# Performance work log

Hardware: AMD Instinct MI355X
Metric: run time of the kernel (lower is better)

Reference implementation:

```python
import jax, jax.numpy as jnp
import numpy as np

N_NODES = 50000
N_EDGES = 800000
N_GRAPHS = 128
IN_DIM = 100
HID = 256
STEPS = 5


def setup_inputs() -> dict:
    key = jax.random.key(0)
    ks = jax.random.split(key, 24)
    s = 0.05
    inp = {
        'x': jax.random.normal(ks[0], (N_NODES, IN_DIM), jnp.float32),
        'edge_index': jax.random.randint(ks[1], (2, N_EDGES), 0, N_NODES, jnp.int32),
        'batch': jnp.sort(jax.random.randint(ks[2], (N_NODES,), 0, N_GRAPHS, jnp.int32)),
        # input projection
        'W_in': jax.random.normal(ks[3], (IN_DIM, HID), jnp.float32) * s,
        'b_in': jnp.zeros((HID,), jnp.float32),
        # GatedGraphConv per-step weights [steps, HID, HID]
        'ggc_w': jax.random.normal(ks[4], (STEPS, HID, HID), jnp.float32) * s,
        # GRUCell params (torch layout: rows = [r, z, n] chunks)
        'W_ih': jax.random.normal(ks[5], (3 * HID, HID), jnp.float32) * s,
        'W_hh': jax.random.normal(ks[6], (3 * HID, HID), jnp.float32) * s,
        'b_ih': jnp.zeros((3 * HID,), jnp.float32),
        'b_hh': jnp.zeros((3 * HID,), jnp.float32),
        # attention MLP: HID -> HID//2 -> 1 (sigmoid)
        'Wa1': jax.random.normal(ks[7], (HID, HID // 2), jnp.float32) * s,
        'ba1': jnp.zeros((HID // 2,), jnp.float32),
        'Wa2': jax.random.normal(ks[8], (HID // 2, 1), jnp.float32) * s,
        'ba2': jnp.zeros((1,), jnp.float32),
        # classifier: 2*HID -> HID -> HID//2 -> 2
        'Wc1': jax.random.normal(ks[9], (2 * HID, HID), jnp.float32) * s,
        'bc1': jnp.zeros((HID,), jnp.float32),
        'Wc2': jax.random.normal(ks[10], (HID, HID // 2), jnp.float32) * s,
        'bc2': jnp.zeros((HID // 2,), jnp.float32),
        'Wc3': jax.random.normal(ks[11], (HID // 2, 2), jnp.float32) * s,
        'bc3': jnp.zeros((2,), jnp.float32),
    }
    return inp


def _forward(x, edge_index, batch, W_in, b_in, ggc_w, W_ih, W_hh, b_ih, b_hh,
             Wa1, ba1, Wa2, ba2, Wc1, bc1, Wc2, bc2, Wc3, bc3):
    src, dst = edge_index[0], edge_index[1]
    # input projection + relu
    h = jax.nn.relu(x @ W_in + b_in)  # [N, HID]

    def ggc_step(h, w):
        m = h @ w                                   # [N, HID]
        agg = jax.ops.segment_sum(m[src], dst, num_segments=N_NODES)  # scatter-add
        gi = agg @ W_ih.T + b_ih                    # [N, 3*HID]
        gh = h @ W_hh.T + b_hh
        i_r, i_z, i_n = jnp.split(gi, 3, axis=-1)
        h_r, h_z, h_n = jnp.split(gh, 3, axis=-1)
        r = jax.nn.sigmoid(i_r + h_r)
        z = jax.nn.sigmoid(i_z + h_z)
        n = jnp.tanh(i_n + r * h_n)
        return (1.0 - z) * n + z * h, None

    h, _ = jax.lax.scan(ggc_step, h, ggc_w)
    h = jax.nn.relu(h)

    # attention weights per node (dropout is identity at eval)
    a = jax.nn.sigmoid(jax.nn.relu(h @ Wa1 + ba1) @ Wa2 + ba2)[:, 0]  # [N]
    wx = h * a[:, None]

    counts = jax.ops.segment_sum(jnp.ones((N_NODES,), h.dtype), batch, num_segments=N_GRAPHS)
    mean_p = jax.ops.segment_sum(wx, batch, num_segments=N_GRAPHS) / jnp.maximum(counts, 1.0)[:, None]
    max_p = jax.ops.segment_max(wx, batch, num_segments=N_GRAPHS)
    max_p = jnp.where(counts[:, None] > 0, max_p, 0.0)
    g = jnp.concatenate([mean_p, max_p], axis=1)  # [G, 2*HID]

    g = jax.nn.relu(g @ Wc1 + bc1)
    g = jax.nn.relu(g @ Wc2 + bc2)
    preds = g @ Wc3 + bc3
    return preds, a


def reference(x, edge_index, batch, W_in, b_in, ggc_w, W_ih, W_hh, b_ih, b_hh,
              Wa1, ba1, Wa2, ba2, Wc1, bc1, Wc2, bc2, Wc3, bc3):
    return _forward(x, edge_index, batch, W_in, b_in, ggc_w, W_ih, W_hh, b_ih, b_hh,
                    Wa1, ba1, Wa2, ba2, Wc1, bc1, Wc2, bc2, Wc3, bc3)
```

## Files before the change

### kernel.cpp

```cpp
#include <hip/hip_runtime.h>
#include <cstddef>

#define NN 50000
#define NE 800000
#define NG 128
#define IND 100
#define HID 256
#define NSTEPS 5
#define PCH 8

typedef __attribute__((ext_vector_type(8))) short bf16x8;
typedef __attribute__((ext_vector_type(4))) float f32x4;

__device__ __forceinline__ float b2f(unsigned h) { return __uint_as_float(h << 16); }
__device__ __forceinline__ unsigned short f2b(float f) {
    unsigned u = __float_as_uint(f);
    unsigned r = (u + 0x7FFFu + ((u >> 16) & 1u)) >> 16;
    return (unsigned short)r;
}
__device__ __forceinline__ float sigm(float x) { return 1.f / (1.f + __expf(-x)); }
__device__ __forceinline__ float tanh_fast(float x) { return 1.f - 2.f / (1.f + __expf(2.f * x)); }

#define LSTR 40
__global__ __launch_bounds__(256) void gemm_bf16(const unsigned short* __restrict__ A,
                                                 const unsigned short* __restrict__ Bt,
                                                 const float* __restrict__ bias, int act,
                                                 unsigned short* __restrict__ C,
                                                 unsigned short* __restrict__ Clo,
                                                 int M, int N, int K,
                                                 size_t btz, size_t cz)
{
    Bt += (size_t)blockIdx.z * btz;
    C  += (size_t)blockIdx.z * cz;
    __shared__ unsigned short As[128 * LSTR];
    __shared__ unsigned short Bs[128 * LSTR];
    const int tid  = threadIdx.x;
    const int row0 = blockIdx.y * 128;
    const int col0 = blockIdx.x * 128;
    const int wave = tid >> 6, lane = tid & 63;
    const int wm = wave >> 1, wn = wave & 1;
    const int lr = lane & 15, q = lane >> 4;
    const int r_st = tid >> 2;
    const int ks   = tid & 3;

    f32x4 acc[4][4];
    #pragma unroll
    for (int i = 0; i < 4; ++i)
        #pragma unroll
        for (int j = 0; j < 4; ++j) acc[i][j] = (f32x4){0.f, 0.f, 0.f, 0.f};

    for (int k0 = 0; k0 < K; k0 += 32) {
        #pragma unroll
        for (int it = 0; it < 2; ++it) {
            int r  = r_st + it * 64;
            int ga = min(row0 + r, M - 1);
            uint4 av = *(const uint4*)(A + (size_t)ga * K + k0 + ks * 8);
            *(uint4*)(As + r * LSTR + ks * 8) = av;
            uint4 bv = *(const uint4*)(Bt + (size_t)(col0 + r) * K + k0 + ks * 8);
            *(uint4*)(Bs + r * LSTR + ks * 8) = bv;
        }
        __syncthreads();
        bf16x8 af[4], bfr[4];
        #pragma unroll
        for (int i = 0; i < 4; ++i)
            af[i]  = *(const bf16x8*)(As + (wm * 64 + i * 16 + lr) * LSTR + q * 8);
        #pragma unroll
        for (int j = 0; j < 4; ++j)
            bfr[j] = *(const bf16x8*)(Bs + (wn * 64 + j * 16 + lr) * LSTR + q * 8);
        #pragma unroll
        for (int i = 0; i < 4; ++i)
            #pragma unroll
            for (int j = 0; j < 4; ++j)
                acc[i][j] = __builtin_amdgcn_mfma_f32_16x16x32_bf16(af[i], bfr[j], acc[i][j], 0, 0, 0);
        __syncthreads();
    }
    #pragma unroll
    for (int i = 0; i < 4; ++i) {
        int rbase = row0 + wm * 64 + i * 16 + q * 4;
        #pragma unroll
        for (int j = 0; j < 4; ++j) {
            int col = col0 + wn * 64 + j * 16 + lr;
            if (col >= N) continue;
            float badd = bias ? bias[col] : 0.f;
            #pragma unroll
            for (int r = 0; r < 4; ++r) {
                int row = rbase + r;
                if (row < M) {
                    float v = acc[i][j][r] + badd;
                    if (act) v = fmaxf(v, 0.f);
                    unsigned short hi = f2b(v);
                    C[(size_t)row * N + col] = hi;
                    if (Clo) Clo[(size_t)row * N + col] = f2b(v - b2f(hi));
                }
            }
        }
    }
}

__global__ __launch_bounds__(256, 4) void gru_mfma(const unsigned short* __restrict__ agg,
                                                   const unsigned short* __restrict__ hbf,
                                                   const unsigned short* __restrict__ hlo,
                                                   unsigned short* __restrict__ hbfo,
                                                   unsigned short* __restrict__ hloo,
                                                   const unsigned short* __restrict__ Wgi,
                                                   const unsigned short* __restrict__ Wgh,
                                                   const float* __restrict__ bih,
                                                   const float* __restrict__ bhh,
                                                   int M, int dorelu)
{
    __shared__ unsigned short Sa[2][64 * LSTR];
    __shared__ unsigned short Sh[2][64 * LSTR];
    const int tid  = threadIdx.x;
    const int row0 = blockIdx.y * 64;
    const int col0 = blockIdx.x * 64;
    const int wave = tid >> 6, lane = tid & 63;
    const int lr = lane & 15, q = lane >> 4;
    const int cw = col0 + wave * 16;
    const int r_st = tid >> 2, ks = tid & 3;

    f32x4 acc[4][4];
    #pragma unroll
    for (int g = 0; g < 4; ++g)
        #pragma unroll
        for (int i = 0; i < 4; ++i) acc[g][i] = (f32x4){0.f, 0.f, 0.f, 0.f};

    const int ga = min(row0 + r_st, M - 1);
    const size_t ab = (size_t)ga * HID + ks * 8;
    {
        uint4 a0 = *(const uint4*)(agg + ab);
        uint4 h0 = *(const uint4*)(hbf + ab);
        *(uint4*)(Sa[0] + r_st * LSTR + ks * 8) = a0;
        *(uint4*)(Sh[0] + r_st * LSTR + ks * 8) = h0;
    }
    uint4 pa = *(const uint4*)(agg + ab + 32);
    uint4 ph = *(const uint4*)(hbf + ab + 32);

    #pragma unroll
    for (int kk = 0; kk < 8; ++kk) {
        const int cur = kk & 1;
        const int k0 = kk * 32;
        __syncthreads();
        if (kk < 7) {
            *(uint4*)(Sa[cur ^ 1] + r_st * LSTR + ks * 8) = pa;
            *(uint4*)(Sh[cur ^ 1] + r_st * LSTR + ks * 8) = ph;
        }
        if (kk < 6) {
            pa = *(const uint4*)(agg + ab + k0 + 64);
            ph = *(const uint4*)(hbf + ab + k0 + 64);
        }
        bf16x8 wir = *(const bf16x8*)(Wgi + (size_t)(0*HID + cw + lr) * HID + k0 + q * 8);
        bf16x8 wiz = *(const bf16x8*)(Wgi + (size_t)(1*HID + cw + lr) * HID + k0 + q * 8);
        bf16x8 win = *(const bf16x8*)(Wgi + (size_t)(2*HID + cw + lr) * HID + k0 + q * 8);
        bf16x8 whr = *(const bf16x8*)(Wgh + (size_t)(0*HID + cw + lr) * HID + k0 + q * 8);
        bf16x8 whz = *(const bf16x8*)(Wgh + (size_t)(1*HID + cw + lr) * HID + k0 + q * 8);
        bf16x8 whn = *(const bf16x8*)(Wgh + (size_t)(2*HID + cw + lr) * HID + k0 + q * 8);
        bf16x8 afa[4], afh[4];
        #pragma unroll
        for (int i = 0; i < 4; ++i) {
            afa[i] = *(const bf16x8*)(Sa[cur] + (i * 16 + lr) * LSTR + q * 8);
            afh[i] = *(const bf16x8*)(Sh[cur] + (i * 16 + lr) * LSTR + q * 8);
        }
        #pragma unroll
        for (int i = 0; i < 4; ++i) {
            acc[0][i] = __builtin_amdgcn_mfma_f32_16x16x32_bf16(afa[i], wir, acc[0][i], 0, 0, 0);
            acc[0][i] = __builtin_amdgcn_mfma_f32_16x16x32_bf16(afh[i], whr, acc[0][i], 0, 0, 0);
            acc[1][i] = __builtin_amdgcn_mfma_f32_16x16x32_bf16(afa[i], wiz, acc[1][i], 0, 0, 0);
            acc[1][i] = __builtin_amdgcn_mfma_f32_16x16x32_bf16(afh[i], whz, acc[1][i], 0, 0, 0);
            acc[2][i] = __builtin_amdgcn_mfma_f32_16x16x32_bf16(afa[i], win, acc[2][i], 0, 0, 0);
            acc[3][i] = __builtin_amdgcn_mfma_f32_16x16x32_bf16(afh[i], whn, acc[3][i], 0, 0, 0);
        }
    }

    const int cg = cw + lr;
    const float brr = bih[cg]         + bhh[cg];
    const float bzz = bih[HID + cg]   + bhh[HID + cg];
    const float bin = bih[2*HID + cg];
    const float bhn = bhh[2*HID + cg];
    #pragma unroll
    for (int i = 0; i < 4; ++i) {
        #pragma unroll
        for (int r = 0; r < 4; ++r) {
            int row = row0 + i * 16 + q * 4 + r;
            if (row < M) {
                float rr = sigm(acc[0][i][r] + brr);
                float zz = sigm(acc[1][i][r] + bzz);
                float nn = tanh_fast(acc[2][i][r] + bin + rr * (acc[3][i][r] + bhn));
                size_t off = (size_t)row * HID + cg;
                float hv = b2f(hbf[off]) + b2f(hlo[off]);
                float o = (1.f - zz) * nn + zz * hv;
                if (dorelu) o = fmaxf(o, 0.f);
                unsigned short hi = f2b(o);
                hbfo[off] = hi;
                hloo[off] = f2b(o - b2f(hi));
            }
        }
    }
}

template<int ACT>
__global__ __launch_bounds__(256) void gemm_kn(const float* __restrict__ A,
                                               const float* __restrict__ B,
                                               const float* __restrict__ bias,
                                               float* __restrict__ C,
                                               int M, int N, int K)
{
    __shared__ float As[64][17];
    __shared__ float Bs[16][65];
    const int tid  = threadIdx.x;
    const int row0 = blockIdx.y * 64;
    const int col0 = blockIdx.x * 64;
    const int tr = tid >> 4, tc = tid & 15;
    const int ar = tid >> 2, akq = tid & 3;
    const int bk = tid >> 4, bj = (tid & 15) << 2;

    float acc[4][4] = {};
    for (int k0 = 0; k0 < K; k0 += 16) {
        float4 av = make_float4(0.f,0.f,0.f,0.f);
        if (row0 + ar < M && (k0 + (akq<<2)) < K)
            av = *(const float4*)(A + (size_t)(row0+ar)*K + k0 + (akq<<2));
        As[ar][(akq<<2)+0] = av.x; As[ar][(akq<<2)+1] = av.y;
        As[ar][(akq<<2)+2] = av.z; As[ar][(akq<<2)+3] = av.w;
        float4 bv = make_float4(0.f,0.f,0.f,0.f);
        if (k0 + bk < K)
            bv = *(const float4*)(B + (size_t)(k0+bk)*N + col0 + bj);
        Bs[bk][bj+0] = bv.x; Bs[bk][bj+1] = bv.y; Bs[bk][bj+2] = bv.z; Bs[bk][bj+3] = bv.w;
        __syncthreads();
        #pragma unroll
        for (int k = 0; k < 16; ++k) {
            float a4[4], b4[4];
            #pragma unroll
            for (int i = 0; i < 4; ++i) a4[i] = As[(tr<<2)+i][k];
            #pragma unroll
            for (int j = 0; j < 4; ++j) b4[j] = Bs[k][(tc<<2)+j];
            #pragma unroll
            for (int i = 0; i < 4; ++i)
                #pragma unroll
                for (int j = 0; j < 4; ++j) acc[i][j] += a4[i]*b4[j];
        }
        __syncthreads();
    }
    #pragma unroll
    for (int i = 0; i < 4; ++i) {
        int row = row0 + (tr<<2) + i;
        if (row >= M) continue;
        #pragma unroll
        for (int j = 0; j < 4; ++j) {
            int col = col0 + (tc<<2) + j;
            float v = acc[i][j];
            if (bias) v += bias[col];
            if (ACT == 1) v = fmaxf(v, 0.f);
            C[(size_t)row*N + col] = v;
        }
    }
}

__global__ void edge_count(const int* __restrict__ dst, int* __restrict__ cnt, int E) {
    int e = blockIdx.x*256 + threadIdx.x;
    if (e < E) atomicAdd(&cnt[dst[e]], 1);
}
__global__ void scan_bsums(const int* __restrict__ cnt, int* __restrict__ bsum, int n) {
    __shared__ int sd[512];
    int tid = threadIdx.x, i = blockIdx.x*512 + tid;
    sd[tid] = (i < n) ? cnt[i] : 0;
    __syncthreads();
    for (int off = 256; off > 0; off >>= 1) {
        if (tid < off) sd[tid] += sd[tid+off];
        __syncthreads();
    }
    if (tid == 0) bsum[blockIdx.x] = sd[0];
}
__global__ void scan_top(int* __restrict__ bsum, int nb) {
    __shared__ int sd[128];
    int tid = threadIdx.x;
    int v = (tid < nb) ? bsum[tid] : 0;
    sd[tid] = v;
    __syncthreads();
    for (int off = 1; off < 128; off <<= 1) {
        int t = (tid >= off) ? sd[tid-off] : 0;
        __syncthreads();
        sd[tid] += t;
        __syncthreads();
    }
    if (tid < nb) bsum[tid] = sd[tid] - v;
}
__global__ void scan_local(const int* __restrict__ cnt, const int* __restrict__ bsum,
                           int* __restrict__ rp, int n) {
    __shared__ int sd[512];
    int tid = threadIdx.x, i = blockIdx.x*512 + tid;
    int v = (i < n) ? cnt[i] : 0;
    sd[tid] = v;
    __syncthreads();
    for (int off = 1; off < 512; off <<= 1) {
        int t = (tid >= off) ? sd[tid-off] : 0;
        __syncthreads();
        sd[tid] += t;
        __syncthreads();
    }
    if (i < n) rp[i] = bsum[blockIdx.x] + sd[tid] - v;
    if (i == n-1) rp[n] = bsum[blockIdx.x] + sd[tid];
}
__global__ void edge_fill(const int* __restrict__ src, const int* __restrict__ dst,
                          const int* __restrict__ rp, int* __restrict__ cur,
                          int* __restrict__ ci, int E) {
    int e = blockIdx.x*256 + threadIdx.x;
    if (e < E) {
        int d = dst[e];
        int pos = rp[d] + atomicAdd(&cur[d], 1);
        ci[pos] = src[e];
    }
}

__global__ void gather_agg(const unsigned short* __restrict__ m, unsigned short* __restrict__ agg,
                           const int* __restrict__ rp, const int* __restrict__ ci, int M)
{
    int node = blockIdx.x*4 + (threadIdx.x >> 6);
    int lane = threadIdx.x & 63;
    if (node >= M) return;
    const int half = lane >> 5;
    const int li   = lane & 31;
    const int s = rp[node], e = rp[node+1];
    float a[8] = {0.f,0.f,0.f,0.f,0.f,0.f,0.f,0.f};
    int cidx[8];
    #pragma unroll
    for (int u = 0; u < 8; ++u) {
        int idx = s + 2*u + half;
        cidx[u] = (idx < e) ? ci[idx] : -1;
    }
    for (int p = s; p < e; p += 16) {
        uint4 v[8];
        #pragma unroll
        for (int u = 0; u < 8; ++u)
            v[u] = (cidx[u] >= 0) ? *(const uint4*)(m + (size_t)cidx[u] * HID + li * 8)
                                  : make_uint4(0u, 0u, 0u, 0u);
        #pragma unroll
        for (int u = 0; u < 8; ++u) {
            int idx = p + 16 + 2*u + half;
            cidx[u] = (idx < e) ? ci[idx] : -1;
        }
        #pragma unroll
        for (int u = 0; u < 8; ++u) {
            a[0] += b2f(v[u].x & 0xffffu); a[1] += b2f(v[u].x >> 16);
            a[2] += b2f(v[u].y & 0xffffu); a[3] += b2f(v[u].y >> 16);
            a[4] += b2f(v[u].z & 0xffffu); a[5] += b2f(v[u].z >> 16);
            a[6] += b2f(v[u].w & 0xffffu); a[7] += b2f(v[u].w >> 16);
        }
    }
    #pragma unroll
    for (int u = 0; u < 8; ++u) a[u] += __shfl_xor(a[u], 32, 64);
    if (half == 0) {
        uint4 o;
        o.x = (unsigned)f2b(a[0]) | ((unsigned)f2b(a[1]) << 16);
        o.y = (unsigned)f2b(a[2]) | ((unsigned)f2b(a[3]) << 16);
        o.z = (unsigned)f2b(a[4]) | ((unsigned)f2b(a[5]) << 16);
        o.w = (unsigned)f2b(a[6]) | ((unsigned)f2b(a[7]) << 16);
        *(uint4*)(agg + (size_t)node * HID + li * 8) = o;
    }
}

__global__ void split_x(const float* __restrict__ x, unsigned short* __restrict__ A) {
    int n = blockIdx.x, k = threadIdx.x;
    unsigned short hi = 0, lo = 0;
    if (k < IND) {
        float v = x[(size_t)n * IND + k];
        hi = f2b(v);
        lo = f2b(v - b2f(hi));
    }
    A[(size_t)n * 256 + k]       = hi;
    A[(size_t)n * 256 + 128 + k] = lo;
}
__global__ void prep_win(const float* __restrict__ w, unsigned short* __restrict__ bt) {
    int n = blockIdx.x, k = threadIdx.x;
    unsigned short v = (k < IND) ? f2b(w[(size_t)k * HID + n]) : (unsigned short)0;
    bt[(size_t)n * 256 + k]       = v;
    bt[(size_t)n * 256 + 128 + k] = v;
}

__global__ void cvt_elem(const float* __restrict__ src, unsigned short* __restrict__ dst, int n) {
    int i = blockIdx.x*256 + threadIdx.x;
    if (i < n) dst[i] = f2b(src[i]);
}
__global__ void prep_wa1(const float* __restrict__ w, unsigned short* __restrict__ wt) {
    int n = blockIdx.x, k = threadIdx.x;
    wt[(size_t)n*HID + k] = f2b(w[(size_t)k*128 + n]);
}

__global__ void att_sig(const unsigned short* __restrict__ t, const float* __restrict__ Wa2,
                        const float* __restrict__ ba2, float* __restrict__ a, int M)
{
    int node = blockIdx.x*4 + (threadIdx.x >> 6);
    int lane = threadIdx.x & 63;
    if (node >= M) return;
    float s = b2f(t[(size_t)node*128 + lane])*Wa2[lane]
            + b2f(t[(size_t)node*128 + 64 + lane])*Wa2[64+lane];
    #pragma unroll
    for (int off = 32; off > 0; off >>= 1) s += __shfl_down(s, off, 64);
    if (lane == 0) a[node] = 1.f/(1.f+__expf(-(s + ba2[0])));
}

__device__ __forceinline__ int lowerb(const int* arr, int n, int val) {
    int lo = 0, hi = n;
    while (lo < hi) { int mid = (lo+hi)>>1; if (arr[mid] < val) lo = mid+1; else hi = mid; }
    return lo;
}
__global__ void pool_partial(const unsigned short* __restrict__ hbf, const float* __restrict__ a,
                             const int* __restrict__ batch, float* __restrict__ part, int M)
{
    int g = blockIdx.x, c = blockIdx.y, j = threadIdx.x;
    int lo = lowerb(batch, M, g);
    int hi = lowerb(batch, M, g+1);
    int len = hi - lo, per = (len + PCH - 1) / PCH;
    int s = lo + c * per, e = min(s + per, hi);
    float sum = 0.f, mx = 0.f;
    for (int n = s; n < e; ++n) {
        float v = b2f(hbf[(size_t)n*HID + j]) * a[n];
        sum += v; mx = fmaxf(mx, v);
    }
    float* pp = part + ((size_t)g*PCH + c) * 512;
    pp[j] = sum; pp[256 + j] = mx;
}
__global__ void pool_final(const float* __restrict__ part, const int* __restrict__ batch,
                           float* __restrict__ gout, int M)
{
    int g = blockIdx.x, j = threadIdx.x;
    float sum = 0.f, mx = 0.f;
    for (int c = 0; c < PCH; ++c) {
        const float* pp = part + ((size_t)g*PCH + c) * 512;
        sum += pp[j];
        mx = fmaxf(mx, pp[256 + j]);
    }
    int lo = lowerb(batch, M, g);
    int hi = lowerb(batch, M, g+1);
    float cnt = (float)(hi - lo);
    gout[(size_t)g*512 + j]       = sum / fmaxf(cnt, 1.f);
    gout[(size_t)g*512 + 256 + j] = mx;
}

__global__ void preds_kernel(const float* __restrict__ g2, const float* __restrict__ W,
                             const float* __restrict__ b, float* __restrict__ out)
{
    int t = threadIdx.x;
    int row = t >> 1, col = t & 1;
    float s = b[col];
    for (int k = 0; k < 128; ++k) s += g2[row*128 + k] * W[k*2 + col];
    out[row*2 + col] = s;
}

extern "C" void kernel_launch(void* const* d_in, const int* in_sizes, int n_in,
                              void* d_out, int out_size, void* d_ws, size_t ws_size,
                              hipStream_t stream)
{
    const float* x     = (const float*)d_in[0];
    const int*   eidx  = (const int*)  d_in[1];
    const int*   batch = (const int*)  d_in[2];
    const float* W_in  = (const float*)d_in[3];
    const float* b_in  = (const float*)d_in[4];
    const float* ggc_w = (const float*)d_in[5];
    const float* W_ih  = (const float*)d_in[6];
    const float* W_hh  = (const float*)d_in[7];
    const float* b_ih  = (const float*)d_in[8];
    const float* b_hh  = (const float*)d_in[9];
    const float* Wa1   = (const float*)d_in[10];
    const float* ba1   = (const float*)d_in[11];
    const float* Wa2   = (const float*)d_in[12];
    const float* ba2   = (const float*)d_in[13];
    const float* Wc1   = (const float*)d_in[14];
    const float* bc1   = (const float*)d_in[15];
    const float* Wc2   = (const float*)d_in[16];
    const float* bc2   = (const float*)d_in[17];
    const float* Wc3   = (const float*)d_in[18];
    const float* bc3   = (const float*)d_in[19];

    float* out  = (float*)d_out;
    float* aout = out + NG*2;

    char* p = (char*)d_ws;
    auto alloc = [&](size_t bytes) -> char* {
        char* r = p; p += (bytes + 255) & ~(size_t)255; return r;
    };
    unsigned short* hbfP  = (unsigned short*)alloc((size_t)NN*HID*2);
    unsigned short* hbfQ  = (unsigned short*)alloc((size_t)NN*HID*2);
    unsigned short* hloP  = (unsigned short*)alloc((size_t)NN*HID*2);
    unsigned short* hloQ  = (unsigned short*)alloc((size_t)NN*HID*2);
    unsigned short* aggbf = (unsigned short*)alloc((size_t)NN*HID*2);
    int* row_ptr = (int*)alloc((NN+1)*4);
    int* cursor  = (int*)alloc(NN*4);
    int* col_idx = (int*)alloc((size_t)NE*4);
    int* bsum    = (int*)alloc(128*4);
    unsigned short* wgbf   = (unsigned short*)alloc((size_t)NSTEPS*HID*HID*2);
    unsigned short* WihBf  = (unsigned short*)alloc((size_t)768*HID*2);
    unsigned short* WhhBf  = (unsigned short*)alloc((size_t)768*HID*2);
    unsigned short* WcombT = (unsigned short*)alloc((size_t)NSTEPS*768*HID*2);
    unsigned short* Wa1t   = (unsigned short*)alloc((size_t)128*HID*2);
    unsigned short* WinT   = (unsigned short*)alloc((size_t)256*256*2);
    float* part = (float*)alloc((size_t)NG*PCH*512*4);
    float* gbuf = (float*)alloc((size_t)NG*2*HID*4);
    float* g1   = (float*)alloc((size_t)NG*HID*4);
    float* g2   = (float*)alloc((size_t)NG*128*4);

    const int* esrc = eidx;
    const int* edst = eidx + NE;
    dim3 blk(256);
    const int NB512 = (NN + 511) / 512;

    hipMemsetAsync(cursor, 0, NN*sizeof(int), stream);
    edge_count<<<NE/256, blk, 0, stream>>>(edst, cursor, NE);
    scan_bsums<<<NB512, 512, 0, stream>>>(cursor, bsum, NN);
    scan_top<<<1, 128, 0, stream>>>(bsum, NB512);
    scan_local<<<NB512, 512, 0, stream>>>(cursor, bsum, row_ptr, NN);
    hipMemsetAsync(cursor, 0, NN*sizeof(int), stream);
    edge_fill<<<NE/256, blk, 0, stream>>>(esrc, edst, row_ptr, cursor, col_idx, NE);

    cvt_elem<<<(NSTEPS*HID*HID + 255)/256, blk, 0, stream>>>(ggc_w, wgbf, NSTEPS*HID*HID);
    cvt_elem<<<768, blk, 0, stream>>>(W_ih, WihBf, 768*HID);
    cvt_elem<<<768, blk, 0, stream>>>(W_hh, WhhBf, 768*HID);
    prep_wa1<<<128, blk, 0, stream>>>(Wa1, Wa1t);
    gemm_bf16<<<dim3(2, 6, NSTEPS), blk, 0, stream>>>(
        WihBf, wgbf, nullptr, 0, WcombT, nullptr, 768, HID, HID,
        (size_t)HID*HID, (size_t)768*HID);

    unsigned short* Ax = hbfQ;
    split_x<<<NN, 128, 0, stream>>>(x, Ax);
    prep_win<<<256, 128, 0, stream>>>(W_in, WinT);
    gemm_bf16<<<dim3(2, (NN+127)/128), blk, 0, stream>>>(
        Ax, WinT, b_in, 1, hbfP, hloP, NN, HID, 256, 0, 0);

    unsigned short* hbf  = hbfP;  unsigned short* hlo  = hloP;
    unsigned short* hbfn = hbfQ;  unsigned short* hlon = hloQ;
    const int MB64 = (NN + 63) / 64;
    for (int s = 0; s < NSTEPS; ++s) {
        gather_agg<<<NN/4, blk, 0, stream>>>(hbf, aggbf, row_ptr, col_idx, NN);
        gru_mfma<<<dim3(HID/64, MB64), blk, 0, stream>>>(
            aggbf, hbf, hlo, hbfn, hlon, WcombT + (size_t)s*768*HID, WhhBf, b_ih, b_hh,
            NN, (s == NSTEPS-1) ? 1 : 0);
        { unsigned short* t0 = hbf; hbf = hbfn; hbfn = t0; }
        { unsigned short* t1 = hlo; hlo = hlon; hlon = t1; }
    }

    unsigned short* tbuf = aggbf;
    gemm_bf16<<<dim3(1, (NN+127)/128), blk, 0, stream>>>(hbf, Wa1t, ba1, 1, tbuf, nullptr, NN, 128, HID, 0, 0);
    att_sig<<<NN/4, blk, 0, stream>>>(tbuf, Wa2, ba2, aout, NN);

    pool_partial<<<dim3(NG, PCH), blk, 0, stream>>>(hbf, aout, batch, part, NN);
    pool_final<<<NG, blk, 0, stream>>>(part, batch, gbuf, NN);

    gemm_kn<1><<<dim3(HID/64, (NG+63)/64), blk, 0, stream>>>(gbuf, Wc1, bc1, g1, NG, HID, 2*HID);
    gemm_kn<1><<<dim3(2,      (NG+63)/64), blk, 0, stream>>>(g1,   Wc2, bc2, g2, NG, 128, HID);
    preds_kernel<<<1, blk, 0, stream>>>(g2, Wc3, bc3, out);
}
```

Baseline: 1.188 ms.

## Widen GRU tile to 128 columns with 512-thread blocks sharing A tiles

The GRU MFMA kernel now runs 8 waves per block covering 128 output columns instead of 4 waves over 64, halving the grid in the column dimension. Each thread stages one of the agg or h tiles rather than both, so the shared A/H tiles are loaded once and reused by twice as many waves. This cuts redundant global reads of agg and h, at the cost of larger blocks that may limit occupancy under the launch-bounds hint of 4 blocks per CU.

```diff
diff --git a/kernel.cpp b/kernel.cpp
--- a/kernel.cpp
+++ b/kernel.cpp
@@ -97,7 +97,7 @@
     }
 }
 
-__global__ __launch_bounds__(256, 4) void gru_mfma(const unsigned short* __restrict__ agg,
+__global__ __launch_bounds__(512, 4) void gru_mfma(const unsigned short* __restrict__ agg,
                                                    const unsigned short* __restrict__ hbf,
                                                    const unsigned short* __restrict__ hlo,
                                                    unsigned short* __restrict__ hbfo,
@@ -112,11 +112,13 @@
     __shared__ unsigned short Sh[2][64 * LSTR];
     const int tid  = threadIdx.x;
     const int row0 = blockIdx.y * 64;
-    const int col0 = blockIdx.x * 64;
+    const int col0 = blockIdx.x * 128;
     const int wave = tid >> 6, lane = tid & 63;
     const int lr = lane & 15, q = lane >> 4;
     const int cw = col0 + wave * 16;
-    const int r_st = tid >> 2, ks = tid & 3;
+    const int r_st = tid >> 3;
+    const int sel  = (tid >> 2) & 1;
+    const int ks   = tid & 3;
 
     f32x4 acc[4][4];
     #pragma unroll
@@ -126,28 +128,21 @@
 
     const int ga = min(row0 + r_st, M - 1);
     const size_t ab = (size_t)ga * HID + ks * 8;
-    {
-        uint4 a0 = *(const uint4*)(agg + ab);
-        uint4 h0 = *(const uint4*)(hbf + ab);
-        *(uint4*)(Sa[0] + r_st * LSTR + ks * 8) = a0;
-        *(uint4*)(Sh[0] + r_st * LSTR + ks * 8) = h0;
-    }
-    uint4 pa = *(const uint4*)(agg + ab + 32);
-    uint4 ph = *(const uint4*)(hbf + ab + 32);
+    const unsigned short* srcp = sel ? hbf : agg;
+    unsigned short* S0 = sel ? Sh[0] : Sa[0];
+    unsigned short* S1 = sel ? Sh[1] : Sa[1];
+    *(uint4*)(S0 + r_st * LSTR + ks * 8) = *(const uint4*)(srcp + ab);
+    uint4 pv = *(const uint4*)(srcp + ab + 32);
 
     #pragma unroll
     for (int kk = 0; kk < 8; ++kk) {
         const int cur = kk & 1;
         const int k0 = kk * 32;
         __syncthreads();
-        if (kk < 7) {
-            *(uint4*)(Sa[cur ^ 1] + r_st * LSTR + ks * 8) = pa;
-            *(uint4*)(Sh[cur ^ 1] + r_st * LSTR + ks * 8) = ph;
-        }
-        if (kk < 6) {
-            pa = *(const uint4*)(agg + ab + k0 + 64);
-            ph = *(const uint4*)(hbf + ab + k0 + 64);
-        }
+        if (kk < 7)
+            *(uint4*)((cur ? S0 : S1) + r_st * LSTR + ks * 8) = pv;
+        if (kk < 6)
+            pv = *(const uint4*)(srcp + ab + k0 + 64);
         bf16x8 wir = *(const bf16x8*)(Wgi + (size_t)(0*HID + cw + lr) * HID + k0 + q * 8);
         bf16x8 wiz = *(const bf16x8*)(Wgi + (size_t)(1*HID + cw + lr) * HID + k0 + q * 8);
         bf16x8 win = *(const bf16x8*)(Wgi + (size_t)(2*HID + cw + lr) * HID + k0 + q * 8);
@@ -529,7 +524,7 @@
     const int MB64 = (NN + 63) / 64;
     for (int s = 0; s < NSTEPS; ++s) {
         gather_agg<<<NN/4, blk, 0, stream>>>(hbf, aggbf, row_ptr, col_idx, NN);
-        gru_mfma<<<dim3(HID/64, MB64), blk, 0, stream>>>(
+        gru_mfma<<<dim3(HID/128, MB64), dim3(512), 0, stream>>>(
             aggbf, hbf, hlo, hbfn, hlon, WcombT + (size_t)s*768*HID, WhhBf, b_ih, b_hh,
             NN, (s == NSTEPS-1) ? 1 : 0);
         { unsigned short* t0 = hbf; hbf = hbfn; hbfn = t0; }
```

Measured after the change: 1.206 ms. Within noise of the previous version (+1.5%).
